# Kernel tuning notes

Measured on AMD Instinct MI355X. Metric: run time of the kernel, lower is better.

Reference implementation:

```python
import jax, jax.numpy as jnp
import numpy as np

TWO_PI = 2.0 * np.pi


def conv2d_circ(x, w, b):
    # x: [B,C,H,W], w: [O,I,3,3]; periodic (circular) padding as used on lattices
    xp = jnp.pad(x, ((0, 0), (0, 0), (1, 1), (1, 1)), mode='wrap')
    y = jax.lax.conv_general_dilated(xp, w, (1, 1), 'VALID',
                                     dimension_numbers=('NCHW', 'OIHW', 'NCHW'))
    return y + b[None, :, None, None]


def setup_inputs() -> dict:
    key = jax.random.key(0)
    ks = jax.random.split(key, 5)
    B, L = 16, 256
    n_bins, hidden = 8, 32  # n_knots = 9
    x = jax.random.uniform(ks[0], (B, L, L), jnp.float32, 0.0, TWO_PI)
    # partition of lattice sites into active / frozen / passive
    ii, jj = np.meshgrid(np.arange(L), np.arange(L), indexing='ij')
    r = (ii % 2) * 2 + (jj % 2)
    active = jnp.asarray((r == 0).astype(np.float32))
    frozen = jnp.asarray(((r == 1) | (r == 2)).astype(np.float32))
    passive = jnp.asarray((r == 3).astype(np.float32))
    conv1_w = 0.1 * jax.random.normal(ks[1], (hidden, 2, 3, 3), jnp.float32)
    conv1_b = 0.01 * jax.random.normal(ks[2], (hidden,), jnp.float32)
    conv2_w = 0.05 * jax.random.normal(ks[3], (3 * n_bins + 1, hidden, 3, 3), jnp.float32)
    conv2_b = 0.01 * jax.random.normal(ks[4], (3 * n_bins + 1,), jnp.float32)
    return {"x": x, "active": active, "frozen": frozen, "passive": passive,
            "conv1_w": conv1_w, "conv1_b": conv1_b, "conv2_w": conv2_w, "conv2_b": conv2_b}


def reference(x, active, frozen, passive, conv1_w, conv1_b, conv2_w, conv2_b):
    n_bins = (conv2_w.shape[0] - 1) // 3
    # prepare_u1_input: conditioner sees only frozen plaquettes, as (cos, sin)
    p2 = frozen * x
    net_in = jnp.stack([jnp.cos(p2), jnp.sin(p2)], axis=1)            # [B,2,L,L]
    h = jax.nn.gelu(conv2d_circ(net_in, conv1_w, conv1_b))
    net_out = conv2d_circ(h, conv2_w, conv2_b)                        # [B,3*nb+1,L,L]
    w = jax.nn.softmax(net_out[:, :n_bins], axis=1)                   # bin widths (sum 1)
    hh = jax.nn.softmax(net_out[:, n_bins:2 * n_bins], axis=1)        # bin heights (sum 1)
    d = jax.nn.softplus(net_out[:, 2 * n_bins:3 * n_bins])            # positive derivatives
    t = net_out[:, -1]                                                # translation, [B,L,L]
    # circular knots on [0, 2pi]
    z = jnp.zeros_like(w[:, :1])
    kx = jnp.concatenate([z, TWO_PI * jnp.cumsum(w, axis=1)], axis=1).at[:, -1].set(TWO_PI)
    ky = jnp.concatenate([z, TWO_PI * jnp.cumsum(hh, axis=1)], axis=1).at[:, -1].set(TWO_PI)
    s = jnp.concatenate([d, d[:, :1]], axis=1)                        # circular: s[K-1]=s[0]
    # dir = 0 (forward pass of the coupling)
    x1 = active * jnp.mod(x, TWO_PI)
    # bin index: count interior knots <= x
    idx = jnp.clip(jnp.sum(kx[:, 1:-1] <= x1[:, None], axis=1), 0, n_bins - 1)[:, None]
    g = lambda a, i: jnp.take_along_axis(a, i, axis=1)[:, 0]
    xk, xk1 = g(kx, idx), g(kx, idx + 1)
    yk, yk1 = g(ky, idx), g(ky, idx + 1)
    dk, dk1 = g(s, idx), g(s, idx + 1)
    wk, hk = xk1 - xk, yk1 - yk
    sl = hk / wk                                                      # bin slope
    th = (x1 - xk) / wk
    th1 = th * (1.0 - th)
    den = sl + (dk1 + dk - 2.0 * sl) * th1
    fx1 = yk + hk * (sl * th * th + dk * th1) / den                   # RQ spline value
    deriv = sl * sl * (dk1 * th * th + 2.0 * sl * th1 + dk * (1.0 - th) ** 2) / (den * den)
    fx1 = active * fx1
    logJ = jnp.sum(active * jnp.log(deriv), axis=(1, 2))              # [B]
    fx = active * jnp.mod(fx1 + t, TWO_PI) + passive * x + frozen * x
    return fx, logJ
```

## Files before the change

### kernel.cpp

```cpp
#include <hip/hip_runtime.h>
#include <hip/hip_bf16.h>

#define TWO_PI 6.283185307179586f

typedef __attribute__((ext_vector_type(8))) short short8;
typedef __attribute__((ext_vector_type(4))) float f32x4;
typedef __attribute__((ext_vector_type(4))) unsigned u32x4;

__device__ __forceinline__ unsigned pack2_bf16(float lo, float hi) {
    return __builtin_amdgcn_perm(__float_as_uint(hi) + 0x8000u,
                                 __float_as_uint(lo) + 0x8000u,
                                 0x07060302u);
}
__device__ __forceinline__ unsigned short f2bf16(float f) {
    return (unsigned short)((__float_as_uint(f) + 0x8000u) >> 16);
}
__device__ __forceinline__ float bf162f(unsigned short h) {
    return __uint_as_float(((unsigned)h) << 16);
}
__device__ __forceinline__ float exp2_raw(float z) {
    float e; asm("v_exp_f32 %0, %1" : "=v"(e) : "v"(z)); return e;
}
__device__ __forceinline__ float log2_raw(float z) {
    float e; asm("v_log_f32 %0, %1" : "=v"(e) : "v"(z)); return e;
}
__device__ __forceinline__ float sin_rev(float rv) {
    float s; asm("v_sin_f32 %0, %1" : "=v"(s) : "v"(rv)); return s;
}
__device__ __forceinline__ float cos_rev(float rv) {
    float c; asm("v_cos_f32 %0, %1" : "=v"(c) : "v"(rv)); return c;
}
#define INV_2PI 0.15915494309189535f
#define LOG2E   1.4426950408889634f
#define LN2     0.6931471805599453f

__device__ __forceinline__ float gelu_fast(float a) {
    float a2 = a * a;
    float p  = __builtin_fmaf(a2, -0.10295206f, -2.3022947928f);
    float e  = exp2_raw(a * p);
    return a * __builtin_amdgcn_rcpf(1.0f + e);
}

__global__ void prep_weights(const float* __restrict__ w1,
                             const float* __restrict__ w2,
                             unsigned short* __restrict__ ws) {
    int t = blockIdx.x * 256 + threadIdx.x;
    if (t >= 10240) return;
    float f = 0.0f;
    if (t < 1024) {
        int o = t >> 5, k = t & 31;
        int ch = (o < 16) ? 2 * o : 2 * (o - 16) + 1;
        if (k < 18) f = w1[ch * 18 + (k & 1) * 9 + (k >> 1)];
    } else {
        int idx = t - 1024;
        int q  = idx >> 10;
        int r  = idx & 1023;
        int cb = r >> 8;
        int o  = (r >> 3) & 31;
        int ci = r & 7;
        if (o < 25) f = w2[(o * 32 + cb * 8 + ci) * 9 + q];
    }
    unsigned a = __float_as_uint(f);
    ws[t] = (unsigned short)((a + 0x7fffu + ((a >> 16) & 1)) >> 16);
}

__global__ void reduce_logj(const float* __restrict__ partial,
                            float* __restrict__ logj) {
    const int bb = threadIdx.x >> 6, i = threadIdx.x & 63;
    const float* p = partial + bb * 256;
    float s = p[i] + p[64 + i] + p[128 + i] + p[192 + i];
    #pragma unroll
    for (int off = 32; off > 0; off >>= 1)
        s += __shfl_down(s, off);
    if (i == 0) logj[bb] = s;
}

#define NO2 30
#define NPOS 578

__global__ __launch_bounds__(512, 6) void plaq_fused(
    const float* __restrict__ x,
    const float* __restrict__ b1, const float* __restrict__ b2,
    const unsigned short* __restrict__ ws,
    float* __restrict__ fx_out, float* __restrict__ partial)
{
    const int tid = threadIdx.x;
    const int bb  = blockIdx.z;
    const int gi0 = blockIdx.y * 16;
    const int gj0 = blockIdx.x * 32;

    __shared__ float xs[20][36];
    __shared__ __align__(16) union {
        unsigned cssn[720];
        unsigned short net_out[128 * NO2];
    } sm;
    __shared__ __align__(16) unsigned hs_u32[NPOS * 16];

    const float* xb = x + (size_t)bb * 65536;

    for (int t = tid; t < 720; t += 512) {
        int r = t / 36, c = t - (t / 36) * 36;
        int gr = (gi0 + r - 2) & 255, gc = (gj0 + c - 2) & 255;
        float v = xb[gr * 256 + gc];
        xs[r][c] = v;
        unsigned pk;
        if ((gr ^ gc) & 1) {
            float rv = v * INV_2PI;
            pk = pack2_bf16(cos_rev(rv), sin_rev(rv));
        } else pk = 0x3f80u;
        sm.cssn[t] = pk;
    }
    __syncthreads();

    const int w  = tid >> 6;
    const int l  = tid & 63;
    const int lg = l >> 4;
    const int lr = l & 15;

    const int sw   = (blockIdx.x + blockIdx.y + blockIdx.z) & 7;
    const int role = (w - sw) & 7;

    if (role >= 2) {
        const int idx3   = role - 2;
        const int off_id = idx3 >> 1;
        const int sub    = ((idx3 & 1) << 6) + l;
        const int oi = 2 * (sub >> 4) + ((off_id + 1) >> 1);
        const int oj = 2 * (sub & 15) + (off_id == 1 ? 0 : 1);
        fx_out[(size_t)bb * 65536 + (gi0 + oi) * 256 + gj0 + oj] = xs[oi + 2][oj + 2];
    }

    {
        short8 bf0 = *(const short8*)(ws + (lr * 32 + lg * 8));
        short8 bf1 = *(const short8*)(ws + ((16 + lr) * 32 + lg * 8));
        const float bias0 = b1[2 * lr], bias1 = b1[2 * lr + 1];

        int offv[4];
        #pragma unroll
        for (int i = 0; i < 4; ++i) {
            int t = lg * 4 + i;
            offv[i] = (t <= 8) ? (t / 3) * 36 + t - (t / 3) * 3 : 0;
        }

        int pr  = w * 16 + lr;
        int hpj = pr % 34;
        int rb  = pr + 2 * (pr / 34);

        unsigned sb[4];
        #pragma unroll
        for (int r = 0; r < 4; ++r) {
            int low6 = lg * 16 + r * 4 + (lr >> 2);
            int xorv = (lg << 1) | (r >> 1);
            sb[r] = (unsigned)(((low6 ^ xorv) * 16) + (lr & 3) * 4 + w * 1024);
        }
        char* hsb = (char*)hs_u32;

        #pragma unroll
        for (int it = 0; it < 5; ++it) {
            if (it < 4 || w < 5) {
                u32x4 aw;
                #pragma unroll
                for (int i = 0; i < 4; ++i) aw[i] = sm.cssn[rb + offv[i]];
                short8 af = __builtin_bit_cast(short8, aw);

                f32x4 d0 = (f32x4){bias0, bias0, bias0, bias0};
                f32x4 d1 = (f32x4){bias1, bias1, bias1, bias1};
                d0 = __builtin_amdgcn_mfma_f32_16x16x32_bf16(af, bf0, d0, 0, 0, 0);
                d1 = __builtin_amdgcn_mfma_f32_16x16x32_bf16(af, bf1, d1, 0, 0, 0);

                #pragma unroll
                for (int r = 0; r < 4; ++r) {
                    if (it < 4 || w < 4 || (lg == 0 && r < 2)) {
                        unsigned pk = pack2_bf16(gelu_fast(d0[r]), gelu_fast(d1[r]));
                        *(unsigned*)(hsb + sb[r] + it * 8192) = pk;
                    }
                }
                hpj += 26; rb += 134;
                if (hpj >= 34) { hpj -= 34; rb += 2; }
            }
        }
    }
    __syncthreads();

    {
        const unsigned short* wt = ws + 1024;
        const int sb2 = w * 272 + lr * 8 + lg;
        float bv0 = b2[lr];
        float bv1 = (lr < 9) ? b2[16 + lr] : 0.0f;
        f32x4 acc0 = (f32x4){bv0, bv0, bv0, bv0};
        f32x4 acc1 = (f32x4){bv1, bv1, bv1, bv1};

        #pragma unroll
        for (int di = 0; di < 3; ++di) {
            #pragma unroll
            for (int dj = 0; dj < 3; ++dj) {
                int q = di * 3 + dj;
                short8 b0  = *(const short8*)(wt + ((q * 4 + lg) * 32 + lr) * 8);
                short8 b1v = *(const short8*)(wt + ((q * 4 + lg) * 32 + 16 + lr) * 8);
                int slot = sb2 + di * 136 + dj * 4;
                slot ^= (slot >> 3) & 7;
                short8 af = *(const short8*)&hs_u32[slot * 4];
                acc0 = __builtin_amdgcn_mfma_f32_16x16x32_bf16(af, b0,  acc0, 0, 0, 0);
                acc1 = __builtin_amdgcn_mfma_f32_16x16x32_bf16(af, b1v, acc1, 0, 0, 0);
            }
        }
        #pragma unroll
        for (int r = 0; r < 4; ++r) {
            int p = 16 * w + 4 * lg + r;
            sm.net_out[p * NO2 + lr] = f2bf16(acc0[r]);
            if (lr < 9) sm.net_out[p * NO2 + 16 + lr] = f2bf16(acc1[r]);
        }
    }
    __syncthreads();

    if (role < 2) {
        const int a  = role * 64 + l;
        const int oi = 2 * (a >> 4), oj = 2 * (a & 15);
        const float xv = xs[oi + 2][oj + 2];

        float no[25];
        #pragma unroll
        for (int ch = 0; ch < 25; ++ch) no[ch] = bf162f(sm.net_out[a * NO2 + ch]);

        float kx[9], ky[9], sa[9];
        {
            float ev[8]; float sum = 0.f;
            #pragma unroll
            for (int k = 0; k < 8; ++k) { ev[k] = exp2_raw(no[k] * LOG2E); sum += ev[k]; }
            float inv = TWO_PI / sum;
            float run = 0.f;
            kx[0] = 0.f;
            #pragma unroll
            for (int k = 0; k < 8; ++k) { run += ev[k]; kx[k + 1] = run * inv; }
            kx[8] = TWO_PI;
        }
        {
            float ev[8]; float sum = 0.f;
            #pragma unroll
            for (int k = 0; k < 8; ++k) { ev[k] = exp2_raw(no[8 + k] * LOG2E); sum += ev[k]; }
            float inv = TWO_PI / sum;
            float run = 0.f;
            ky[0] = 0.f;
            #pragma unroll
            for (int k = 0; k < 8; ++k) { run += ev[k]; ky[k + 1] = run * inv; }
            ky[8] = TWO_PI;
        }
        #pragma unroll
        for (int k = 0; k < 8; ++k) {
            float v = no[16 + k];
            float e = exp2_raw(v * LOG2E);
            sa[k] = (v > 20.f) ? v : LN2 * log2_raw(1.0f + e);
        }
        sa[8] = sa[0];

        float x1 = xv;

        int idx = 0;
        #pragma unroll
        for (int k = 1; k < 8; ++k) idx += (kx[k] <= x1) ? 1 : 0;

        float xk = 0, xk1 = 0, yk = 0, yk1 = 0, dk = 0, dk1 = 0;
        #pragma unroll
        for (int k = 0; k < 9; ++k) {
            if (k == idx)     { xk  = kx[k]; yk  = ky[k]; dk  = sa[k]; }
            if (k == idx + 1) { xk1 = kx[k]; yk1 = ky[k]; dk1 = sa[k]; }
        }

        float wk  = xk1 - xk;
        float hk  = yk1 - yk;
        float sl  = hk / wk;
        float th  = (x1 - xk) / wk;
        float th1 = th * (1.f - th);
        float den = sl + (dk1 + dk - 2.f * sl) * th1;
        float fx1 = yk + hk * (sl * th * th + dk * th1) / den;
        float omt = 1.f - th;
        float deriv = sl * sl * (dk1 * th * th + 2.f * sl * th1 + dk * omt * omt)
                      / (den * den);
        float logd = LN2 * log2_raw(deriv);

        float m = fx1 + no[24];
        if (m >= TWO_PI) m -= TWO_PI;
        if (m < 0.f)     m += TWO_PI;

        fx_out[(size_t)bb * 65536 + (gi0 + oi) * 256 + gj0 + oj] = m;

        #pragma unroll
        for (int off = 32; off > 0; off >>= 1)
            logd += __shfl_down(logd, off);
        if (l == 0) {
            int bid = (bb * 128 + blockIdx.y * 8 + blockIdx.x) * 2 + role;
            partial[bid] = logd;
        }
    }
}

extern "C" void kernel_launch(void* const* d_in, const int* in_sizes, int n_in,
                              void* d_out, int out_size, void* d_ws, size_t ws_size,
                              hipStream_t stream) {
    const float* x  = (const float*)d_in[0];
    const float* w1 = (const float*)d_in[4];
    const float* b1 = (const float*)d_in[5];
    const float* w2 = (const float*)d_in[6];
    const float* b2 = (const float*)d_in[7];

    float* fx_out = (float*)d_out;
    float* logj   = (float*)d_out + (size_t)16 * 256 * 256;
    unsigned short* ws = (unsigned short*)d_ws;
    float* partial = (float*)((char*)d_ws + 20480);

    prep_weights<<<40, 256, 0, stream>>>(w1, w2, ws);

    dim3 grid(8, 16, 16);
    plaq_fused<<<grid, 512, 0, stream>>>(x, b1, b2, ws, fx_out, partial);

    reduce_logj<<<1, 1024, 0, stream>>>(partial, logj);
}
```

Measured before the change: 36.72 us.

## Use 10 waves per block for conv1 and vectorize the tile load

The block grows from 8 to 10 waves. The conv1 (hidden layer) stage now spreads its 578 positions over 10 waves in 4 iterations instead of 8 waves in 5, with the position strides and LDS offsets adjusted to match. The two extra waves sit idle during conv2 and the passthrough stores. The input tile is now loaded as float2 pairs by 360 threads, computing cos/sin once per pair. The occupancy hint changes to (640, 7), which may push registers down or spill.

```diff
diff --git a/kernel.cpp b/kernel.cpp
--- a/kernel.cpp
+++ b/kernel.cpp
@@ -78,7 +78,7 @@
 #define NO2 30
 #define NPOS 578
 
-__global__ __launch_bounds__(512, 6) void plaq_fused(
+__global__ __launch_bounds__(640, 7) void plaq_fused(
     const float* __restrict__ x,
     const float* __restrict__ b1, const float* __restrict__ b2,
     const unsigned short* __restrict__ ws,
@@ -98,17 +98,21 @@
 
     const float* xb = x + (size_t)bb * 65536;
 
-    for (int t = tid; t < 720; t += 512) {
-        int r = t / 36, c = t - (t / 36) * 36;
-        int gr = (gi0 + r - 2) & 255, gc = (gj0 + c - 2) & 255;
-        float v = xb[gr * 256 + gc];
-        xs[r][c] = v;
-        unsigned pk;
-        if ((gr ^ gc) & 1) {
-            float rv = v * INV_2PI;
-            pk = pack2_bf16(cos_rev(rv), sin_rev(rv));
-        } else pk = 0x3f80u;
-        sm.cssn[t] = pk;
+    if (tid < 360) {
+        int r  = tid / 18, cp = tid - (tid / 18) * 18;
+        int c0 = 2 * cp;
+        int gr  = (gi0 + r - 2) & 255;
+        int gc0 = (gj0 + c0 - 2) & 255;
+        float2 v = *(const float2*)(xb + gr * 256 + gc0);
+        *(float2*)&xs[r][c0] = v;
+        int f = (gr ^ gc0) & 1;
+        float xv = f ? v.x : v.y;
+        float rv = xv * INV_2PI;
+        unsigned pk = pack2_bf16(cos_rev(rv), sin_rev(rv));
+        uint2 out;
+        out.x = f ? pk : 0x3f80u;
+        out.y = f ? 0x3f80u : pk;
+        *(uint2*)&sm.cssn[r * 36 + c0] = out;
     }
     __syncthreads();
 
@@ -117,10 +121,10 @@
     const int lg = l >> 4;
     const int lr = l & 15;
 
-    const int sw   = (blockIdx.x + blockIdx.y + blockIdx.z) & 7;
-    const int role = (w - sw) & 7;
-
-    if (role >= 2) {
+    const unsigned sblk = (blockIdx.x + blockIdx.y + blockIdx.z) % 10u;
+    int role = w - (int)sblk; if (role < 0) role += 10;
+
+    if (role >= 2 && role < 8) {
         const int idx3   = role - 2;
         const int off_id = idx3 >> 1;
         const int sub    = ((idx3 & 1) << 6) + l;
@@ -155,8 +159,8 @@
         char* hsb = (char*)hs_u32;
 
         #pragma unroll
-        for (int it = 0; it < 5; ++it) {
-            if (it < 4 || w < 5) {
+        for (int it = 0; it < 4; ++it) {
+            if (it < 3 || w < 7) {
                 u32x4 aw;
                 #pragma unroll
                 for (int i = 0; i < 4; ++i) aw[i] = sm.cssn[rb + offv[i]];
@@ -169,19 +173,19 @@
 
                 #pragma unroll
                 for (int r = 0; r < 4; ++r) {
-                    if (it < 4 || w < 4 || (lg == 0 && r < 2)) {
+                    if (it < 3 || w < 6 || (lg == 0 && r < 2)) {
                         unsigned pk = pack2_bf16(gelu_fast(d0[r]), gelu_fast(d1[r]));
-                        *(unsigned*)(hsb + sb[r] + it * 8192) = pk;
+                        *(unsigned*)(hsb + sb[r] + it * 10240) = pk;
                     }
                 }
-                hpj += 26; rb += 134;
+                hpj += 24; rb += 168;
                 if (hpj >= 34) { hpj -= 34; rb += 2; }
             }
         }
     }
     __syncthreads();
 
-    {
+    if (w < 8) {
         const unsigned short* wt = ws + 1024;
         const int sb2 = w * 272 + lr * 8 + lg;
         float bv0 = b2[lr];
@@ -310,7 +314,7 @@
     prep_weights<<<40, 256, 0, stream>>>(w1, w2, ws);
 
     dim3 grid(8, 16, 16);
-    plaq_fused<<<grid, 512, 0, stream>>>(x, b1, b2, ws, fx_out, partial);
+    plaq_fused<<<grid, 640, 0, stream>>>(x, b1, b2, ws, fx_out, partial);
 
     reduce_logj<<<1, 1024, 0, stream>>>(partial, logj);
 }
```

Result: slower. 41.73 us (+13.6%).
